# Kernel optimization log

Hardware: AMD Instinct MI355X
Metric: run time of the kernel (lower is better)

Reference implementation:

```python
import jax, jax.numpy as jnp
import numpy as np
import math

NUM_HEADS = 16
NUM_KV_HEADS = 4
HEAD_DIM = 128
ROPE_THETA = 10000.0


def rotate_half(x):
    half = x.shape[-1] // 2
    return jnp.concatenate((-x[..., half:], x[..., :half]), axis=-1)


def setup_inputs() -> dict:
    key = jax.random.key(0)
    ks = jax.random.split(key, 5)
    B, S, H = 2, 2048, 2048
    hidden_states = jax.random.normal(ks[0], (B, S, H), dtype=jnp.float32)
    scale = 1.0 / math.sqrt(H)
    wq = jax.random.normal(ks[1], (NUM_HEADS * HEAD_DIM, H), dtype=jnp.float32) * scale
    wk = jax.random.normal(ks[2], (NUM_KV_HEADS * HEAD_DIM, H), dtype=jnp.float32) * scale
    wv = jax.random.normal(ks[3], (NUM_KV_HEADS * HEAD_DIM, H), dtype=jnp.float32) * scale
    wo = jax.random.normal(ks[4], (H, NUM_HEADS * HEAD_DIM), dtype=jnp.float32) * scale
    # additive causal mask [B,1,S,S]
    causal = jnp.where(jnp.tril(jnp.ones((S, S), dtype=bool)), 0.0, -1e9).astype(jnp.float32)
    attention_mask = jnp.broadcast_to(causal[None, None], (B, 1, S, S))
    position_ids = jnp.broadcast_to(jnp.arange(S, dtype=jnp.int64)[None], (B, S))
    return {
        'hidden_states': hidden_states, 'wq': wq, 'wk': wk, 'wv': wv, 'wo': wo,
        'attention_mask': attention_mask, 'position_ids': position_ids,
    }


def reference(hidden_states, wq, wk, wv, wo, attention_mask, position_ids):
    B, S, H = hidden_states.shape
    nh, nkv, hd = NUM_HEADS, NUM_KV_HEADS, HEAD_DIM
    groups = nh // nkv

    # projections (torch Linear: x @ W^T)
    q = (hidden_states @ wq.T).reshape(B, S, nh, hd).transpose(0, 2, 1, 3)   # [B,nh,S,hd]
    k = (hidden_states @ wk.T).reshape(B, S, nkv, hd).transpose(0, 2, 1, 3)  # [B,nkv,S,hd]
    v = (hidden_states @ wv.T).reshape(B, S, nkv, hd).transpose(0, 2, 1, 3)

    # RoPE: cos/sin gathered by position_ids -> [B,1,S,hd]
    inv_freq = 1.0 / (ROPE_THETA ** (jnp.arange(0, hd, 2, dtype=jnp.float32) / hd))  # [hd/2]
    freqs = position_ids.astype(jnp.float32)[:, :, None] * inv_freq                  # [B,S,hd/2]
    emb = jnp.concatenate((freqs, freqs), axis=-1)                                   # [B,S,hd]
    cos = jnp.cos(emb)[:, None]
    sin = jnp.sin(emb)[:, None]
    q = q * cos + rotate_half(q) * sin
    k = k * cos + rotate_half(k) * sin

    # GQA: repeat kv heads
    k = jnp.repeat(k, groups, axis=1)  # [B,nh,S,hd]
    v = jnp.repeat(v, groups, axis=1)

    scores = jnp.einsum('bhqd,bhkd->bhqk', q, k) / math.sqrt(hd) + attention_mask
    attn = jax.nn.softmax(scores.astype(jnp.float32), axis=-1).astype(q.dtype)
    ctx = jnp.einsum('bhqk,bhkd->bhqd', attn, v)            # [B,nh,S,hd]
    ctx = ctx.transpose(0, 2, 1, 3).reshape(B, S, nh * hd)  # [B,S,H]
    out = ctx @ wo.T
    return out
```

## Files before the change

### kernel.cpp

```cpp
#include <hip/hip_runtime.h>
#include <hip/hip_bf16.h>
#include <stdint.h>

typedef __bf16 bf16x8 __attribute__((ext_vector_type(8)));
typedef float f32x4 __attribute__((ext_vector_type(4)));
typedef float f32x16 __attribute__((ext_vector_type(16)));

#define NH 16
#define NKV 4
#define HD 128
#define HQ (NH*HD)
#define HKV (NKV*HD)
#define LDX 3072

__device__ __forceinline__ void gl_lds16(const void* g, void* l) {
  __builtin_amdgcn_global_load_lds(
      (const __attribute__((address_space(1))) void*)g,
      (__attribute__((address_space(3))) void*)l, 16, 0, 0);
}

__device__ __forceinline__ uint32_t pk2(float lo, float hi) {
  union { __hip_bfloat16 h[2]; uint32_t u; } x;
  x.h[0] = __float2bfloat16(lo);
  x.h[1] = __float2bfloat16(hi);
  return x.u;
}

__global__ void k_cast_all(const float* __restrict__ hs, const float* __restrict__ wq,
                           const float* __restrict__ wk, const float* __restrict__ wv,
                           const float* __restrict__ wo,
                           __hip_bfloat16* __restrict__ Xb, __hip_bfloat16* __restrict__ Wqb,
                           __hip_bfloat16* __restrict__ Wkb, __hip_bfloat16* __restrict__ Wvb,
                           __hip_bfloat16* __restrict__ Wob) {
  int i = blockIdx.x * blockDim.x + threadIdx.x;
  const float* src; __hip_bfloat16* dst; int off;
  if (i < 2097152)      { src = hs; dst = Xb;  off = i; }
  else if (i < 3145728) { src = wq; dst = Wqb; off = i - 2097152; }
  else if (i < 3407872) { src = wk; dst = Wkb; off = i - 3145728; }
  else if (i < 3670016) { src = wv; dst = Wvb; off = i - 3407872; }
  else                  { src = wo; dst = Wob; off = i - 3670016; }
  float4 v = reinterpret_cast<const float4*>(src)[off];
  union { __hip_bfloat16 b[4]; ushort4 u; } o;
  o.b[0] = __float2bfloat16(v.x); o.b[1] = __float2bfloat16(v.y);
  o.b[2] = __float2bfloat16(v.z); o.b[3] = __float2bfloat16(v.w);
  reinterpret_cast<ushort4*>(dst)[off] = o.u;
}

__global__ void k_rope_vt(__hip_bfloat16* __restrict__ X, __hip_bfloat16* __restrict__ Vt,
                          const int* __restrict__ pid, int S) {
  __shared__ __hip_bfloat16 tile[32][33];
  const int RB = 20480;
  if (blockIdx.x < RB) {
    int idx = blockIdx.x * 256 + threadIdx.x;
    int i = idx & 63;
    int hh = (idx >> 6) % 20;
    int tok = idx / (20 * 64);
    bool is64 = (pid[1] == 0);
    int pos = is64 ? pid[2 * tok] : pid[tok];
    float f = (float)pos * __expf(-(float)i * (9.210340371976184f / 64.0f));
    float sn, cs;
    __sincosf(f, &sn, &cs);
    size_t base = (size_t)tok * LDX + hh * 128;
    float x0 = __bfloat162float(X[base + i]);
    float x1 = __bfloat162float(X[base + 64 + i]);
    X[base + i]      = __float2bfloat16(x0 * cs - x1 * sn);
    X[base + 64 + i] = __float2bfloat16(x1 * cs + x0 * sn);
  } else {
    int bb = blockIdx.x - RB;
    int bkv = bb >> 8;
    int rem = bb & 255;
    int s0 = (rem & 63) * 32, d0 = (rem >> 6) * 32;
    int b = bkv >> 2, kvh = bkv & 3;
    int tx = threadIdx.x & 31, ty = threadIdx.x >> 5;
    for (int i = 0; i < 32; i += 8)
      tile[ty + i][tx] = X[((size_t)(b * S) + s0 + ty + i) * LDX + 2560 + kvh * 128 + d0 + tx];
    __syncthreads();
    for (int i = 0; i < 32; i += 8)
      Vt[((size_t)bkv * 128 + d0 + ty + i) * S + s0 + tx] = tile[tx][ty + i];
  }
}

__global__ __launch_bounds__(512, 1) void k_gemmQKV(
    const __hip_bfloat16* __restrict__ A, const __hip_bfloat16* __restrict__ B,
    __hip_bfloat16* __restrict__ C, int Nld, int K) {
  __shared__ __hip_bfloat16 As[2][2][256 * 32];
  __shared__ __hip_bfloat16 Bs[2][2][256 * 32];

  const int t = threadIdx.x, w = t >> 6, l = t & 63;
  const int lr = l & 15, lg = l >> 4;
  const int wr = w >> 2, wc = w & 3;

  const int bid = blockIdx.x;
  const int id2 = (bid & 7) * 24 + (bid >> 3);
  const int bm = id2 & 15, bn = id2 >> 4;

  const __hip_bfloat16* Ap = A + (size_t)(bm * 256) * K;
  const __hip_bfloat16* Bp = B + (size_t)(bn * 256) * K;

  auto stageHalf = [&](const __hip_bfloat16* gp, __hip_bfloat16* lp, int kt, int kk) {
#pragma unroll
    for (int inst = 0; inst < 2; ++inst) {
      const int chunk = inst * 512 + t;
      const int row = chunk >> 2, c_st = chunk & 3;
      const int c_nat = c_st ^ ((row >> 1) & 3);
      gl_lds16(gp + (size_t)row * K + kt * 64 + kk * 32 + c_nat * 8,
               lp + (size_t)(inst * 512 + (w << 6)) * 8);
    }
  };

  f32x4 acc[8][4] = {};
  const int nt = K >> 6;

  stageHalf(Ap, As[0][0], 0, 0);
  stageHalf(Bp, Bs[0][0], 0, 0);
  stageHalf(Ap, As[0][1], 0, 1);
  stageHalf(Bp, Bs[0][1], 0, 1);
  stageHalf(Ap, As[1][0], 1, 0);
  stageHalf(Bp, Bs[1][0], 1, 0);
  asm volatile("s_waitcnt vmcnt(4)" ::: "memory");
  __builtin_amdgcn_s_barrier();
  asm volatile("" ::: "memory");

  for (int tt = 0; tt < nt; ++tt) {
    const int cur = tt & 1;
    const int nx1 = (tt + 1 < nt) ? tt + 1 : nt - 1;
    const int nx2 = (tt + 2 < nt) ? tt + 2 : nt - 1;
    bf16x8 bF[4];
#pragma unroll
    for (int ph = 0; ph < 4; ++ph) {
      const int kk = ph >> 1, mh = ph & 1;
      bf16x8 aF[4];
      if (mh == 0) {
#pragma unroll
        for (int n = 0; n < 4; ++n) {
          int rB = wc * 64 + n * 16 + lr;
          bF[n] = *reinterpret_cast<const bf16x8*>(
              &Bs[cur][kk][rB * 32 + (lg ^ ((rB >> 1) & 3)) * 8]);
        }
      }
#pragma unroll
      for (int m = 0; m < 4; ++m) {
        int rA = wr * 128 + mh * 64 + m * 16 + lr;
        aF[m] = *reinterpret_cast<const bf16x8*>(
            &As[cur][kk][rA * 32 + (lg ^ ((rA >> 1) & 3)) * 8]);
      }
      if (ph == 0)      stageHalf(Ap, As[nx1 & 1][1], nx1, 1);
      else if (ph == 1) stageHalf(Bp, Bs[nx1 & 1][1], nx1, 1);
      else if (ph == 2) stageHalf(Ap, As[nx2 & 1][0], nx2, 0);
      else              stageHalf(Bp, Bs[nx2 & 1][0], nx2, 0);
      asm volatile("" ::: "memory");
      __builtin_amdgcn_s_barrier();
      asm volatile("" ::: "memory");
      __builtin_amdgcn_s_setprio(1);
#pragma unroll
      for (int m = 0; m < 4; ++m)
#pragma unroll
        for (int n = 0; n < 4; ++n)
          acc[mh * 4 + m][n] = __builtin_amdgcn_mfma_f32_16x16x32_bf16(
              aF[m], bF[n], acc[mh * 4 + m][n], 0, 0, 0);
      __builtin_amdgcn_s_setprio(0);
      if (ph == 3) asm volatile("s_waitcnt vmcnt(4)" ::: "memory");
      asm volatile("" ::: "memory");
      __builtin_amdgcn_s_barrier();
      asm volatile("" ::: "memory");
    }
  }

  const int row0 = bm * 256 + wr * 128;
  const int col0 = bn * 256 + wc * 64;
#pragma unroll
  for (int m = 0; m < 8; ++m)
#pragma unroll
    for (int n = 0; n < 4; ++n)
#pragma unroll
      for (int r = 0; r < 4; ++r)
        C[(size_t)(row0 + m * 16 + lg * 4 + r) * Nld + col0 + n * 16 + lr] =
            __float2bfloat16(acc[m][n][r]);
}

__global__ __launch_bounds__(512, 1) void k_gemmO(
    const __hip_bfloat16* __restrict__ A, const __hip_bfloat16* __restrict__ B,
    float* __restrict__ C, int N, int K) {
  __shared__ __hip_bfloat16 As[2][2][128 * 32];
  __shared__ __hip_bfloat16 Bs[2][2][256 * 32];

  const int t = threadIdx.x, w = t >> 6, l = t & 63;
  const int lr = l & 15, lg = l >> 4;
  const int wr = w >> 2, wc = w & 3;

  const int bid = blockIdx.x;
  const int id2 = (bid & 7) * 32 + (bid >> 3);
  const int bm = id2 & 31, bn = id2 >> 5;

  const __hip_bfloat16* Ap = A + (size_t)(bm * 128) * K;
  const __hip_bfloat16* Bp = B + (size_t)(bn * 256) * K;

  auto stageA = [&](__hip_bfloat16* lp, int kt, int kk) {
    const int row = t >> 2, c_st = t & 3;
    const int c_nat = c_st ^ ((row >> 1) & 3);
    gl_lds16(Ap + (size_t)row * K + kt * 64 + kk * 32 + c_nat * 8,
             lp + (size_t)(w << 6) * 8);
  };
  auto stageB = [&](__hip_bfloat16* lp, int kt, int kk) {
#pragma unroll
    for (int inst = 0; inst < 2; ++inst) {
      const int chunk = inst * 512 + t;
      const int row = chunk >> 2, c_st = chunk & 3;
      const int c_nat = c_st ^ ((row >> 1) & 3);
      gl_lds16(Bp + (size_t)row * K + kt * 64 + kk * 32 + c_nat * 8,
               lp + (size_t)(inst * 512 + (w << 6)) * 8);
    }
  };

  f32x4 acc[4][4] = {};
  const int nt = K >> 6;

  stageA(As[0][0], 0, 0);
  stageB(Bs[0][0], 0, 0);
  stageA(As[0][1], 0, 1);
  stageB(Bs[0][1], 0, 1);
  stageA(As[1][0], 1, 0);
  stageB(Bs[1][0], 1, 0);
  asm volatile("s_waitcnt vmcnt(3)" ::: "memory");
  __builtin_amdgcn_s_barrier();
  asm volatile("" ::: "memory");

  for (int tt = 0; tt < nt; ++tt) {
    const int cur = tt & 1;
    const int nx1 = (tt + 1 < nt) ? tt + 1 : nt - 1;
    const int nx2 = (tt + 2 < nt) ? tt + 2 : nt - 1;
    bf16x8 bF[4];
#pragma unroll
    for (int ph = 0; ph < 4; ++ph) {
      const int kk = ph >> 1, mh = ph & 1;
      bf16x8 aF[2];
      if (mh == 0) {
#pragma unroll
        for (int n = 0; n < 4; ++n) {
          int rB = wc * 64 + n * 16 + lr;
          bF[n] = *reinterpret_cast<const bf16x8*>(
              &Bs[cur][kk][rB * 32 + (lg ^ ((rB >> 1) & 3)) * 8]);
        }
      }
#pragma unroll
      for (int m2 = 0; m2 < 2; ++m2) {
        int rA = wr * 64 + mh * 32 + m2 * 16 + lr;
        aF[m2] = *reinterpret_cast<const bf16x8*>(
            &As[cur][kk][rA * 32 + (lg ^ ((rA >> 1) & 3)) * 8]);
      }
      if (ph == 0)      stageA(As[nx1 & 1][1], nx1, 1);
      else if (ph == 1) stageB(Bs[nx1 & 1][1], nx1, 1);
      else if (ph == 2) stageA(As[nx2 & 1][0], nx2, 0);
      else              stageB(Bs[nx2 & 1][0], nx2, 0);
      asm volatile("" ::: "memory");
      __builtin_amdgcn_s_barrier();
      asm volatile("" ::: "memory");
      __builtin_amdgcn_s_setprio(1);
#pragma unroll
      for (int m2 = 0; m2 < 2; ++m2)
#pragma unroll
        for (int n = 0; n < 4; ++n)
          acc[mh * 2 + m2][n] = __builtin_amdgcn_mfma_f32_16x16x32_bf16(
              aF[m2], bF[n], acc[mh * 2 + m2][n], 0, 0, 0);
      __builtin_amdgcn_s_setprio(0);
      if (ph == 3) asm volatile("s_waitcnt vmcnt(3)" ::: "memory");
      asm volatile("" ::: "memory");
      __builtin_amdgcn_s_barrier();
      asm volatile("" ::: "memory");
    }
  }

  const int row0 = bm * 128 + wr * 64;
  const int col0 = bn * 256 + wc * 64;
#pragma unroll
  for (int m = 0; m < 4; ++m)
#pragma unroll
    for (int n = 0; n < 4; ++n)
#pragma unroll
      for (int r = 0; r < 4; ++r)
        C[(size_t)(row0 + m * 16 + lg * 4 + r) * N + col0 + n * 16 + lr] =
            acc[m][n][r];
}

__global__ __launch_bounds__(256, 2) void k_attn(
    const __hip_bfloat16* __restrict__ X, const __hip_bfloat16* __restrict__ Vt,
    __hip_bfloat16* __restrict__ ctx, int S) {
  __shared__ __hip_bfloat16 SM[32768];

  const int bid = blockIdx.x;
  const int g  = bid & 7;
  const int idx = bid >> 3;
  int hi, jj;
  if (idx < 32) { hi = idx >> 4;              jj = idx & 15; }
  else          { hi = 2 + ((idx - 32) >> 4); jj = 15 - ((idx - 32) & 15); }
  const int b = g >> 2, kvh = g & 3;
  const int h = kvh * 4 + hi;

  const int t = threadIdx.x, w = t >> 6, l = t & 63;
  const int q = l & 31, hf = l >> 5;
  const int qt64 = (w < 2) ? jj : (31 - jj);
  const int q0w = qt64 * 64 + (w & 1) * 32;
  const int nt = 32 - jj;
  const float c1 = 0.12752511f;
  const float M0 = 48.0f;

  const __hip_bfloat16* Qp = X + ((size_t)(b * S) + q0w + q) * LDX + h * 128 + hf * 8;
  bf16x8 aq[8];
#pragma unroll
  for (int m = 0; m < 8; ++m)
    aq[m] = *reinterpret_cast<const bf16x8*>(Qp + m * 16);

  const __hip_bfloat16* KG = X + (size_t)(b * S) * LDX + 2048 + kvh * 128;
  const __hip_bfloat16* VG = Vt + ((size_t)(b * NKV + kvh) * 128) * S;

  auto stageK = [&](int buf, int kv0) {
#pragma unroll
    for (int j = 0; j < 4; ++j) {
      int off16 = (w * 4 + j) * 64 + l;
      int row = off16 >> 4;
      int c_nat = (off16 & 15) ^ (row & 7);
      gl_lds16(KG + (size_t)(kv0 + row) * LDX + c_nat * 8,
               &SM[buf * 8192 + (w * 4 + j) * 512]);
    }
  };
  auto stageV = [&](int buf, int kv0) {
#pragma unroll
    for (int j = 0; j < 4; ++j) {
      int off16 = (w * 4 + j) * 64 + l;
      int d = off16 >> 3;
      int c_nat = (off16 & 7) ^ (d & 7);
      gl_lds16(VG + (size_t)d * S + kv0 + c_nat * 8,
               &SM[16384 + buf * 8192 + (w * 4 + j) * 512]);
    }
  };

  f32x16 O[4] = {};
  float l_i = 0.0f;

  stageK(0, 0); stageV(0, 0);
  int cur = 0;
  for (int tkv = 0; tkv < nt; ++tkv) {
    const int kv0 = tkv * 64;
    if (tkv + 1 < nt) {
      stageK(cur ^ 1, kv0 + 64);
      stageV(cur ^ 1, kv0 + 64);
      asm volatile("s_waitcnt vmcnt(8)" ::: "memory");
    } else {
      asm volatile("s_waitcnt vmcnt(0)" ::: "memory");
    }
    __builtin_amdgcn_sched_barrier(0);
    __builtin_amdgcn_s_barrier();
    asm volatile("" ::: "memory");

    if (kv0 <= q0w + 31) {
      const __hip_bfloat16* Ksb = &SM[cur * 8192];
      const __hip_bfloat16* Vsb = &SM[16384 + cur * 8192];

      f32x16 p[2];
      __builtin_amdgcn_s_setprio(1);
#pragma unroll
      for (int sb = 0; sb < 2; ++sb) {
        f32x16 s0 = {}, s1 = {};
#pragma unroll
        for (int mm = 0; mm < 4; ++mm) {
          int arow = sb * 32 + q;
          int c0 = (4 * mm + hf) ^ (arow & 7);
          int c1i = (4 * mm + 2 + hf) ^ (arow & 7);
          bf16x8 kf0 = *reinterpret_cast<const bf16x8*>(&Ksb[arow * 128 + c0 * 8]);
          bf16x8 kf1 = *reinterpret_cast<const bf16x8*>(&Ksb[arow * 128 + c1i * 8]);
          s0 = __builtin_amdgcn_mfma_f32_32x32x16_bf16(kf0, aq[2 * mm], s0, 0, 0, 0);
          s1 = __builtin_amdgcn_mfma_f32_32x32x16_bf16(kf1, aq[2 * mm + 1], s1, 0, 0, 0);
        }
        p[sb] = s0 + s1;
      }
      __builtin_amdgcn_s_setprio(0);

      if (kv0 + 63 > q0w) {
#pragma unroll
        for (int sb = 0; sb < 2; ++sb)
#pragma unroll
          for (int r = 0; r < 16; ++r) {
            int kv_abs = kv0 + sb * 32 + (r & 3) + 8 * (r >> 2) + 4 * hf;
            if (kv_abs > q0w + q) p[sb][r] = -3.0e38f;
          }
      }

      float rs = 0.0f;
#pragma unroll
      for (int sb = 0; sb < 2; ++sb)
#pragma unroll
        for (int r = 0; r < 16; ++r) {
          float e = exp2f((p[sb][r] - M0) * c1);
          p[sb][r] = e;
          rs += e;
        }
      rs += __shfl_xor(rs, 32, 64);
      l_i += rs;

      uint32_t pku[2][8], swu[2][8];
#pragma unroll
      for (int sb = 0; sb < 2; ++sb)
#pragma unroll
        for (int gp = 0; gp < 4; ++gp) {
          pku[sb][gp * 2 + 0] = pk2(p[sb][gp * 4 + 0], p[sb][gp * 4 + 1]);
          pku[sb][gp * 2 + 1] = pk2(p[sb][gp * 4 + 2], p[sb][gp * 4 + 3]);
        }
#pragma unroll
      for (int sb = 0; sb < 2; ++sb)
#pragma unroll
        for (int ii = 0; ii < 8; ++ii)
          swu[sb][ii] = __shfl_xor((int)pku[sb][ii], 32, 64);

      __builtin_amdgcn_s_setprio(1);
#pragma unroll
      for (int kk = 0; kk < 4; ++kk) {
        const int sb = kk >> 1, bs = (kk & 1) * 4;
        union { uint32_t u[4]; bf16x8 v; } pf;
        pf.u[0] = hf ? swu[sb][bs + 2] : pku[sb][bs + 0];
        pf.u[1] = hf ? swu[sb][bs + 3] : pku[sb][bs + 1];
        pf.u[2] = hf ? pku[sb][bs + 2] : swu[sb][bs + 0];
        pf.u[3] = hf ? pku[sb][bs + 3] : swu[sb][bs + 1];
#pragma unroll
        for (int db = 0; db < 4; ++db) {
          int vrow = db * 32 + q;
          int c_lds = (2 * kk + hf) ^ (vrow & 7);
          bf16x8 vf = *reinterpret_cast<const bf16x8*>(&Vsb[vrow * 64 + c_lds * 8]);
          O[db] = __builtin_amdgcn_mfma_f32_32x32x16_bf16(vf, pf.v, O[db], 0, 0, 0);
        }
      }
      __builtin_amdgcn_s_setprio(0);
    }
    asm volatile("" ::: "memory");
    __builtin_amdgcn_s_barrier();
    asm volatile("" ::: "memory");
    cur ^= 1;
  }

  float inv = 1.0f / l_i;
  __hip_bfloat16* Lo = &SM[w * 4352];
#pragma unroll
  for (int db = 0; db < 4; ++db)
#pragma unroll
    for (int rr = 0; rr < 4; ++rr) {
      int d0 = db * 32 + rr * 8 + hf * 4;
      uint32_t u0 = pk2(O[db][rr * 4 + 0] * inv, O[db][rr * 4 + 1] * inv);
      uint32_t u1 = pk2(O[db][rr * 4 + 2] * inv, O[db][rr * 4 + 3] * inv);
      *reinterpret_cast<uint2*>(&Lo[q * 136 + d0]) = make_uint2(u0, u1);
    }
  __syncthreads();
#pragma unroll
  for (int it = 0; it < 8; ++it) {
    int row = it * 4 + (l >> 4), c = l & 15;
    bf16x8 vv = *reinterpret_cast<const bf16x8*>(&Lo[row * 136 + c * 8]);
    *reinterpret_cast<bf16x8*>(
        &ctx[((size_t)(b * S) + q0w + row) * HQ + h * 128 + c * 8]) = vv;
  }
}

extern "C" void kernel_launch(void* const* d_in, const int* in_sizes, int n_in,
                              void* d_out, int out_size, void* d_ws, size_t ws_size,
                              hipStream_t stream) {
  const int B = 2, S = 2048, H = 2048;
  const int M = B * S;

  const float* hs = (const float*)d_in[0];
  const float* wq = (const float*)d_in[1];
  const float* wk = (const float*)d_in[2];
  const float* wv = (const float*)d_in[3];
  const float* wo = (const float*)d_in[4];
  const int* pid = (const int*)d_in[6];

  char* p = (char*)d_ws;
  auto carve = [&](size_t bytes) {
    void* r = (void*)p;
    p += (bytes + 255) & ~(size_t)255;
    return r;
  };
  __hip_bfloat16* Xb   = (__hip_bfloat16*)carve((size_t)M * H * 2);
  __hip_bfloat16* Wqb  = (__hip_bfloat16*)carve((size_t)HQ * H * 2);
  __hip_bfloat16* Wkb  = (__hip_bfloat16*)carve((size_t)HKV * H * 2);
  __hip_bfloat16* Wvb  = (__hip_bfloat16*)carve((size_t)HKV * H * 2);
  __hip_bfloat16* Wob  = (__hip_bfloat16*)carve((size_t)H * HQ * 2);
  __hip_bfloat16* XQKV = (__hip_bfloat16*)carve((size_t)M * LDX * 2);
  __hip_bfloat16* Vtb  = (__hip_bfloat16*)carve((size_t)M * HKV * 2);
  __hip_bfloat16* Ctx  = (__hip_bfloat16*)carve((size_t)M * HQ * 2);

  k_cast_all<<<18432, 256, 0, stream>>>(hs, wq, wk, wv, wo, Xb, Wqb, Wkb, Wvb, Wob);

  k_gemmQKV<<<dim3(192), 512, 0, stream>>>(Xb, Wqb, XQKV, LDX, H);

  k_rope_vt<<<dim3(20480 + 2048), 256, 0, stream>>>(XQKV, Vtb, pid, S);

  k_attn<<<dim3(512), 256, 0, stream>>>(XQKV, Vtb, Ctx, S);

  k_gemmO<<<dim3(256), 512, 0, stream>>>(Ctx, Wob, (float*)d_out, H, HQ);
}
```

Measured before the change: 249.2 us.

## Fuse Q RoPE into attention kernel and retile QKV GEMM to 256x192

Q-head RoPE moves out of the standalone rope kernel and into the attention kernel, applied to the Q fragments held in registers right after they load. The rope kernel now only rotates K heads, which cuts its grid and the global read/write traffic over the Q section. The QKV GEMM tile shrinks from 256x256 to 256x192 so the grid grows from 192 to 256 blocks, filling the CUs more evenly. In exchange, some waves do uneven B staging with per-wave vmcnt waits, and attention spends extra transcendental work per Q element.

```diff
diff --git a/kernel.cpp b/kernel.cpp
--- a/kernel.cpp
+++ b/kernel.cpp
@@ -49,18 +49,18 @@
 __global__ void k_rope_vt(__hip_bfloat16* __restrict__ X, __hip_bfloat16* __restrict__ Vt,
                           const int* __restrict__ pid, int S) {
   __shared__ __hip_bfloat16 tile[32][33];
-  const int RB = 20480;
+  const int RB = 4096;
   if (blockIdx.x < RB) {
     int idx = blockIdx.x * 256 + threadIdx.x;
     int i = idx & 63;
-    int hh = (idx >> 6) % 20;
-    int tok = idx / (20 * 64);
+    int hh = (idx >> 6) & 3;
+    int tok = idx >> 8;
     bool is64 = (pid[1] == 0);
     int pos = is64 ? pid[2 * tok] : pid[tok];
     float f = (float)pos * __expf(-(float)i * (9.210340371976184f / 64.0f));
     float sn, cs;
     __sincosf(f, &sn, &cs);
-    size_t base = (size_t)tok * LDX + hh * 128;
+    size_t base = (size_t)tok * LDX + 2048 + hh * 128;
     float x0 = __bfloat162float(X[base + i]);
     float x1 = __bfloat162float(X[base + 64 + i]);
     X[base + i]      = __float2bfloat16(x0 * cs - x1 * sn);
@@ -84,40 +84,60 @@
     const __hip_bfloat16* __restrict__ A, const __hip_bfloat16* __restrict__ B,
     __hip_bfloat16* __restrict__ C, int Nld, int K) {
   __shared__ __hip_bfloat16 As[2][2][256 * 32];
-  __shared__ __hip_bfloat16 Bs[2][2][256 * 32];
+  __shared__ __hip_bfloat16 Bs[2][2][192 * 32];
 
   const int t = threadIdx.x, w = t >> 6, l = t & 63;
   const int lr = l & 15, lg = l >> 4;
   const int wr = w >> 2, wc = w & 3;
 
   const int bid = blockIdx.x;
-  const int id2 = (bid & 7) * 24 + (bid >> 3);
+  const int id2 = (bid & 7) * 32 + (bid >> 3);
   const int bm = id2 & 15, bn = id2 >> 4;
 
   const __hip_bfloat16* Ap = A + (size_t)(bm * 256) * K;
-  const __hip_bfloat16* Bp = B + (size_t)(bn * 256) * K;
-
-  auto stageHalf = [&](const __hip_bfloat16* gp, __hip_bfloat16* lp, int kt, int kk) {
+  const __hip_bfloat16* Bp = B + (size_t)(bn * 192) * K;
+
+  auto stageA = [&](__hip_bfloat16* lp, int kt, int kk) {
 #pragma unroll
     for (int inst = 0; inst < 2; ++inst) {
       const int chunk = inst * 512 + t;
       const int row = chunk >> 2, c_st = chunk & 3;
       const int c_nat = c_st ^ ((row >> 1) & 3);
-      gl_lds16(gp + (size_t)row * K + kt * 64 + kk * 32 + c_nat * 8,
+      gl_lds16(Ap + (size_t)row * K + kt * 64 + kk * 32 + c_nat * 8,
                lp + (size_t)(inst * 512 + (w << 6)) * 8);
     }
   };
-
-  f32x4 acc[8][4] = {};
+  auto stageB = [&](__hip_bfloat16* lp, int kt, int kk) {
+    {
+      const int chunk = t;
+      const int row = chunk >> 2, c_st = chunk & 3;
+      const int c_nat = c_st ^ ((row >> 1) & 3);
+      gl_lds16(Bp + (size_t)row * K + kt * 64 + kk * 32 + c_nat * 8,
+               lp + (size_t)(w << 6) * 8);
+    }
+    if (w < 4) {
+      const int chunk = 512 + t;
+      const int row = chunk >> 2, c_st = chunk & 3;
+      const int c_nat = c_st ^ ((row >> 1) & 3);
+      gl_lds16(Bp + (size_t)row * K + kt * 64 + kk * 32 + c_nat * 8,
+               lp + (size_t)(512 + (w << 6)) * 8);
+    }
+  };
+  auto waitTile = [&](int wv) {
+    if (wv < 4) asm volatile("s_waitcnt vmcnt(4)" ::: "memory");
+    else        asm volatile("s_waitcnt vmcnt(3)" ::: "memory");
+  };
+
+  f32x4 acc[8][3] = {};
   const int nt = K >> 6;
 
-  stageHalf(Ap, As[0][0], 0, 0);
-  stageHalf(Bp, Bs[0][0], 0, 0);
-  stageHalf(Ap, As[0][1], 0, 1);
-  stageHalf(Bp, Bs[0][1], 0, 1);
-  stageHalf(Ap, As[1][0], 1, 0);
-  stageHalf(Bp, Bs[1][0], 1, 0);
-  asm volatile("s_waitcnt vmcnt(4)" ::: "memory");
+  stageA(As[0][0], 0, 0);
+  stageB(Bs[0][0], 0, 0);
+  stageA(As[0][1], 0, 1);
+  stageB(Bs[0][1], 0, 1);
+  stageA(As[1][0], 1, 0);
+  stageB(Bs[1][0], 1, 0);
+  waitTile(w);
   __builtin_amdgcn_s_barrier();
   asm volatile("" ::: "memory");
 
@@ -125,15 +145,15 @@
     const int cur = tt & 1;
     const int nx1 = (tt + 1 < nt) ? tt + 1 : nt - 1;
     const int nx2 = (tt + 2 < nt) ? tt + 2 : nt - 1;
-    bf16x8 bF[4];
+    bf16x8 bF[3];
 #pragma unroll
     for (int ph = 0; ph < 4; ++ph) {
       const int kk = ph >> 1, mh = ph & 1;
       bf16x8 aF[4];
       if (mh == 0) {
 #pragma unroll
-        for (int n = 0; n < 4; ++n) {
-          int rB = wc * 64 + n * 16 + lr;
+        for (int n = 0; n < 3; ++n) {
+          int rB = wc * 48 + n * 16 + lr;
           bF[n] = *reinterpret_cast<const bf16x8*>(
               &Bs[cur][kk][rB * 32 + (lg ^ ((rB >> 1) & 3)) * 8]);
         }
@@ -144,10 +164,10 @@
         aF[m] = *reinterpret_cast<const bf16x8*>(
             &As[cur][kk][rA * 32 + (lg ^ ((rA >> 1) & 3)) * 8]);
       }
-      if (ph == 0)      stageHalf(Ap, As[nx1 & 1][1], nx1, 1);
-      else if (ph == 1) stageHalf(Bp, Bs[nx1 & 1][1], nx1, 1);
-      else if (ph == 2) stageHalf(Ap, As[nx2 & 1][0], nx2, 0);
-      else              stageHalf(Bp, Bs[nx2 & 1][0], nx2, 0);
+      if (ph == 0)      stageA(As[nx1 & 1][1], nx1, 1);
+      else if (ph == 1) stageB(Bs[nx1 & 1][1], nx1, 1);
+      else if (ph == 2) stageA(As[nx2 & 1][0], nx2, 0);
+      else              stageB(Bs[nx2 & 1][0], nx2, 0);
       asm volatile("" ::: "memory");
       __builtin_amdgcn_s_barrier();
       asm volatile("" ::: "memory");
@@ -155,11 +175,11 @@
 #pragma unroll
       for (int m = 0; m < 4; ++m)
 #pragma unroll
-        for (int n = 0; n < 4; ++n)
+        for (int n = 0; n < 3; ++n)
           acc[mh * 4 + m][n] = __builtin_amdgcn_mfma_f32_16x16x32_bf16(
               aF[m], bF[n], acc[mh * 4 + m][n], 0, 0, 0);
       __builtin_amdgcn_s_setprio(0);
-      if (ph == 3) asm volatile("s_waitcnt vmcnt(4)" ::: "memory");
+      if (ph == 3) waitTile(w);
       asm volatile("" ::: "memory");
       __builtin_amdgcn_s_barrier();
       asm volatile("" ::: "memory");
@@ -167,15 +187,15 @@
   }
 
   const int row0 = bm * 256 + wr * 128;
-  const int col0 = bn * 256 + wc * 64;
+  const int col0 = bn * 192 + wc * 48;
 #pragma unroll
   for (int m = 0; m < 8; ++m)
 #pragma unroll
-    for (int n = 0; n < 4; ++n)
+    for (int n = 0; n < 3; ++n)
 #pragma unroll
       for (int r = 0; r < 4; ++r)
-        C[(size_t)(row0 + m * 16 + lg * 4 + r) * Nld + col0 + n * 16 + lr] =
-            __float2bfloat16(acc[m][n][r]);
+        C[(size_t)(row0 + (m >> 2) * 64 + (m & 3) * 16 + lg * 4 + r) * Nld +
+          col0 + n * 16 + lr] = __float2bfloat16(acc[m][n][r]);
 }
 
 __global__ __launch_bounds__(512, 1) void k_gemmO(
@@ -284,7 +304,7 @@
 
 __global__ __launch_bounds__(256, 2) void k_attn(
     const __hip_bfloat16* __restrict__ X, const __hip_bfloat16* __restrict__ Vt,
-    __hip_bfloat16* __restrict__ ctx, int S) {
+    const int* __restrict__ pid, __hip_bfloat16* __restrict__ ctx, int S) {
   __shared__ __hip_bfloat16 SM[32768];
 
   const int bid = blockIdx.x;
@@ -309,6 +329,26 @@
 #pragma unroll
   for (int m = 0; m < 8; ++m)
     aq[m] = *reinterpret_cast<const bf16x8*>(Qp + m * 16);
+
+  {
+    bool is64 = (pid[1] == 0);
+    int toki = b * S + q0w + q;
+    int pos = is64 ? pid[2 * toki] : pid[toki];
+    float fpos = (float)pos;
+#pragma unroll
+    for (int mq = 0; mq < 4; ++mq)
+#pragma unroll
+      for (int j = 0; j < 8; ++j) {
+        int fi = mq * 16 + hf * 8 + j;
+        float ang = fpos * __expf((float)fi * (-9.210340371976184f / 64.0f));
+        float sn, cs;
+        __sincosf(ang, &sn, &cs);
+        float x0 = (float)aq[mq][j];
+        float x1 = (float)aq[mq + 4][j];
+        aq[mq][j]     = (__bf16)(x0 * cs - x1 * sn);
+        aq[mq + 4][j] = (__bf16)(x1 * cs + x0 * sn);
+      }
+  }
 
   const __hip_bfloat16* KG = X + (size_t)(b * S) * LDX + 2048 + kvh * 128;
   const __hip_bfloat16* VG = Vt + ((size_t)(b * NKV + kvh) * 128) * S;
@@ -487,11 +527,11 @@
 
   k_cast_all<<<18432, 256, 0, stream>>>(hs, wq, wk, wv, wo, Xb, Wqb, Wkb, Wvb, Wob);
 
-  k_gemmQKV<<<dim3(192), 512, 0, stream>>>(Xb, Wqb, XQKV, LDX, H);
-
-  k_rope_vt<<<dim3(20480 + 2048), 256, 0, stream>>>(XQKV, Vtb, pid, S);
-
-  k_attn<<<dim3(512), 256, 0, stream>>>(XQKV, Vtb, Ctx, S);
+  k_gemmQKV<<<dim3(256), 512, 0, stream>>>(Xb, Wqb, XQKV, LDX, H);
+
+  k_rope_vt<<<dim3(4096 + 2048), 256, 0, stream>>>(XQKV, Vtb, pid, S);
+
+  k_attn<<<dim3(512), 256, 0, stream>>>(XQKV, Vtb, pid, Ctx, S);
 
   k_gemmO<<<dim3(256), 512, 0, stream>>>(Ctx, Wob, (float*)d_out, H, HQ);
 }
```

Measured after the change: 244.6 us. About the same (-1.8%).
